# Kernel tuning notes

Hardware: AMD Instinct MI355X
Metric: run time of the kernel (lower is better)

The kernel has to match this reference:

```python
import jax, jax.numpy as jnp
import numpy as np

V, BLK, D, H, L = 50257, 2048, 768, 12, 4
HD = D // H
EPS = 1e-5


def _ln(x, w, b):
    mu = jnp.mean(x, axis=-1, keepdims=True)
    var = jnp.mean(jnp.square(x - mu), axis=-1, keepdims=True)
    return (x - mu) * jax.lax.rsqrt(var + EPS) * w + b


def setup_inputs() -> dict:
    key = jax.random.key(0)
    ks = iter(jax.random.split(key, 32))
    s = 0.02
    idx = jax.random.randint(next(ks), (2, 2048), 0, V)
    inp = {
        "idx": idx,
        "wte": jax.random.normal(next(ks), (V, D), jnp.float32) * s,
        "wpe": jax.random.normal(next(ks), (BLK, D), jnp.float32) * s,
        # stacked per-layer params [L, ...]
        "ln1_w": jnp.ones((L, D), jnp.float32),
        "ln1_b": jnp.zeros((L, D), jnp.float32),
        "attn_w": jax.random.normal(next(ks), (L, D, 3 * D), jnp.float32) * s,
        "attn_b": jnp.zeros((L, 3 * D), jnp.float32),
        "proj_w": jax.random.normal(next(ks), (L, D, D), jnp.float32) * (s / np.sqrt(2 * L)),
        "proj_b": jnp.zeros((L, D), jnp.float32),
        "ln2_w": jnp.ones((L, D), jnp.float32),
        "ln2_b": jnp.zeros((L, D), jnp.float32),
        "fc_w": jax.random.normal(next(ks), (L, D, 4 * D), jnp.float32) * s,
        "fc_b": jnp.zeros((L, 4 * D), jnp.float32),
        "fcp_w": jax.random.normal(next(ks), (L, 4 * D, D), jnp.float32) * (s / np.sqrt(2 * L)),
        "fcp_b": jnp.zeros((L, D), jnp.float32),
        "lnf_w": jnp.ones((D,), jnp.float32),
        "lnf_b": jnp.zeros((D,), jnp.float32),
    }
    return inp


def _gpt_forward(idx, wte, wpe, ln1_w, ln1_b, attn_w, attn_b, proj_w, proj_b,
                 ln2_w, ln2_b, fc_w, fc_b, fcp_w, fcp_b, lnf_w, lnf_b):
    B, T = idx.shape
    x = wte[idx] + wpe[:T]  # [B,T,D]; dropout p=0 -> identity
    causal = jnp.tril(jnp.ones((T, T), bool))
    scale = 1.0 / np.sqrt(HD)

    def block(x, p):
        l1w, l1b, aw, ab, pw, pb, l2w, l2b, fw, fb, fpw, fpb = p
        h = _ln(x, l1w, l1b)
        qkv = h @ aw + ab  # [B,T,3D]
        q, k, v = jnp.split(qkv, 3, axis=-1)
        q = q.reshape(B, T, H, HD).transpose(0, 2, 1, 3)  # [B,H,T,hd]
        k = k.reshape(B, T, H, HD).transpose(0, 2, 1, 3)
        v = v.reshape(B, T, H, HD).transpose(0, 2, 1, 3)
        att = jnp.einsum('bhqd,bhkd->bhqk', q, k) * scale
        att = jnp.where(causal, att, -jnp.inf)
        att = jax.nn.softmax(att, axis=-1)
        y = jnp.einsum('bhqk,bhkd->bhqd', att, v)
        y = y.transpose(0, 2, 1, 3).reshape(B, T, D)
        x = x + y @ pw + pb
        h2 = _ln(x, l2w, l2b)
        m = jax.nn.gelu(h2 @ fw + fb, approximate=False) @ fpw + fpb
        return x + m, None

    params = (ln1_w, ln1_b, attn_w, attn_b, proj_w, proj_b,
              ln2_w, ln2_b, fc_w, fc_b, fcp_w, fcp_b)
    x, _ = jax.lax.scan(block, x, params)
    x = _ln(x, lnf_w, lnf_b)
    # inference path: logits only for last position, lm_head tied to wte
    logits = x[:, -1:, :] @ wte.T  # [B,1,V]
    return logits


def reference(idx, wte, wpe, ln1_w, ln1_b, attn_w, attn_b, proj_w, proj_b,
              ln2_w, ln2_b, fc_w, fc_b, fcp_w, fcp_b, lnf_w, lnf_b):
    return _gpt_forward(idx, wte, wpe, ln1_w, ln1_b, attn_w, attn_b, proj_w, proj_b,
                        ln2_w, ln2_b, fc_w, fc_b, fcp_w, fcp_b, lnf_w, lnf_b)
```

## Files before the change

### kernel.cpp

```cpp
#include <hip/hip_runtime.h>
#include <math.h>

#define V 50257
#define B 2
#define T 2048
#define D 768
#define H 12
#define HD 64
#define L 4
#define D3 (3*D)
#define D4 (4*D)
#define NTOK (B*T)
#define EPS 1e-5f

typedef __bf16 v8bf __attribute__((ext_vector_type(8)));
typedef unsigned short v8us __attribute__((ext_vector_type(8)));
typedef float  v4f  __attribute__((ext_vector_type(4)));

#define GAS(p) ((const __attribute__((address_space(1))) void*)(p))
#define LAS(p) ((__attribute__((address_space(3))) void*)(p))

#define LIDX(row, chunk) ((row)*64 + ((((chunk) ^ ((row)&7)))<<3))

__global__ __launch_bounds__(256) void embed_kernel(const int* __restrict__ idx,
                                                    const float* __restrict__ wte,
                                                    const float* __restrict__ wpe,
                                                    float* __restrict__ x) {
    int i = blockIdx.x * 256 + threadIdx.x;
    if (i >= NTOK * D) return;
    int pos = i / D;
    int d   = i - pos * D;
    int t   = pos & (T - 1);
    int tok = idx[pos];
    x[i] = wte[tok * D + d] + wpe[t * D + d];
}

__global__ __launch_bounds__(256) void ln_kernel(const float* __restrict__ X,
                                                 const float* __restrict__ w,
                                                 const float* __restrict__ b,
                                                 __bf16* __restrict__ Y,
                                                 int src_mul, int src_off) {
    int srow = blockIdx.x * src_mul + src_off;
    const float* xr = X + (size_t)srow * D;
    float v[3];
    float s = 0.f, s2 = 0.f;
    #pragma unroll
    for (int j = 0; j < 3; ++j) {
        v[j] = xr[threadIdx.x + 256 * j];
        s += v[j];
        s2 += v[j] * v[j];
    }
    #pragma unroll
    for (int off = 32; off; off >>= 1) {
        s  += __shfl_xor(s, off);
        s2 += __shfl_xor(s2, off);
    }
    __shared__ float ss[4], ss2[4];
    int wave = threadIdx.x >> 6, lane = threadIdx.x & 63;
    if (lane == 0) { ss[wave] = s; ss2[wave] = s2; }
    __syncthreads();
    s  = ss[0] + ss[1] + ss[2] + ss[3];
    s2 = ss2[0] + ss2[1] + ss2[2] + ss2[3];
    float mu  = s * (1.f / D);
    float var = s2 * (1.f / D) - mu * mu;
    float rs  = rsqrtf(var + EPS);
    __bf16* yr = Y + (size_t)blockIdx.x * D;
    #pragma unroll
    for (int j = 0; j < 3; ++j) {
        int c = threadIdx.x + 256 * j;
        yr[c] = (__bf16)((v[j] - mu) * rs * w[c] + b[c]);
    }
}

__global__ __launch_bounds__(256) void convw4_kernel(
        const float* __restrict__ aw,  const float* __restrict__ pw,
        const float* __restrict__ fw,  const float* __restrict__ fpw,
        __bf16* __restrict__ awt, __bf16* __restrict__ pwt,
        __bf16* __restrict__ fwt, __bf16* __restrict__ fpwt) {
    int bid = blockIdx.x;
    const float* W; __bf16* Wt; int K, N, bx, by;
    if (bid < 1728)      {             W = aw;  Wt = awt;  K = D;  N = D3; bx = bid % 72; by = bid / 72; }
    else if (bid < 2304) { bid -= 1728; W = pw;  Wt = pwt;  K = D;  N = D;  bx = bid % 24; by = bid / 24; }
    else if (bid < 4608) { bid -= 2304; W = fw;  Wt = fwt;  K = D;  N = D4; bx = bid % 96; by = bid / 96; }
    else                 { bid -= 4608; W = fpw; Wt = fpwt; K = D4; N = D;  bx = bid % 24; by = bid / 24; }
    __shared__ float t[32][33];
    const int n0 = bx * 32, k0 = by * 32;
    const int tx = threadIdx.x & 31, ty = threadIdx.x >> 5;
    #pragma unroll
    for (int p = 0; p < 4; ++p)
        t[ty + 8 * p][tx] = W[(size_t)(k0 + ty + 8 * p) * N + n0 + tx];
    __syncthreads();
    #pragma unroll
    for (int p = 0; p < 4; ++p)
        Wt[(size_t)(n0 + ty + 8 * p) * K + k0 + tx] = (__bf16)t[tx][ty + 8 * p];
}

template<bool OUTBF16, bool DOGELU, bool DORES>
__global__ __launch_bounds__(256) void gemm_bt(const __bf16* __restrict__ A,
                                               const __bf16* __restrict__ Wt,
                                               const float* __restrict__ bias,
                                               const float* __restrict__ res,
                                               void* __restrict__ Cout,
                                               int N, int K) {
    __shared__ __align__(16) __bf16 As[4096];
    __shared__ __align__(16) __bf16 Bs[4096];
    const int tid  = threadIdx.x;
    const int w    = tid >> 6;
    const int lane = tid & 63;
    const int row0 = blockIdx.y * 128;
    const int col0 = blockIdx.x * 128;

    const int c0   = w * 64 + lane;
    const int srow = ((c0 >> 6) & 3) * 16 + (c0 & 15);
    const int sk   = ((c0 >> 4) & 3) * 8;
    const __bf16* gA0 = A  + (size_t)(row0 + srow) * K + sk;
    const __bf16* gA1 = gA0 + (size_t)64 * K;
    const __bf16* gB0 = Wt + (size_t)(col0 + srow) * K + sk;
    const __bf16* gB1 = gB0 + (size_t)64 * K;
    __bf16* lA0 = As + (size_t)c0 * 8;
    __bf16* lA1 = As + (size_t)(c0 + 256) * 8;
    __bf16* lB0 = Bs + (size_t)c0 * 8;
    __bf16* lB1 = Bs + (size_t)(c0 + 256) * 8;

    const int wr = w >> 1, wc = w & 1;
    const __bf16* rA = As + wr * 2048 + lane * 8;
    const __bf16* rB = Bs + wc * 2048 + lane * 8;

    v4f acc[4][4] = {};
    for (int k0 = 0; k0 < K; k0 += 32) {
        __builtin_amdgcn_global_load_lds(GAS(gA0), LAS(lA0), 16, 0, 0);
        __builtin_amdgcn_global_load_lds(GAS(gA1), LAS(lA1), 16, 0, 0);
        __builtin_amdgcn_global_load_lds(GAS(gB0), LAS(lB0), 16, 0, 0);
        __builtin_amdgcn_global_load_lds(GAS(gB1), LAS(lB1), 16, 0, 0);
        gA0 += 32; gA1 += 32; gB0 += 32; gB1 += 32;
        __syncthreads();
        v8bf af[4], bfr[4];
        #pragma unroll
        for (int i = 0; i < 4; ++i) af[i]  = *(const v8bf*)(rA + i * 512);
        #pragma unroll
        for (int j = 0; j < 4; ++j) bfr[j] = *(const v8bf*)(rB + j * 512);
        #pragma unroll
        for (int i = 0; i < 4; ++i)
            #pragma unroll
            for (int j = 0; j < 4; ++j)
                acc[i][j] = __builtin_amdgcn_mfma_f32_16x16x32_bf16(af[i], bfr[j], acc[i][j], 0, 0, 0);
        __syncthreads();
    }

    const int er = (lane >> 4) * 4;
    const int ec = lane & 15;
    #pragma unroll
    for (int j = 0; j < 4; ++j) {
        const int col = col0 + wc * 64 + j * 16 + ec;
        const float bval = bias[col];
        #pragma unroll
        for (int i = 0; i < 4; ++i) {
            #pragma unroll
            for (int rr = 0; rr < 4; ++rr) {
                const int row = row0 + wr * 64 + i * 16 + er + rr;
                float vv = acc[i][j][rr] + bval;
                if (DOGELU) vv = 0.5f * vv * (1.f + erff(vv * 0.70710678118f));
                if (DORES)  vv += res[(size_t)row * N + col];
                if (OUTBF16) ((__bf16*)Cout)[(size_t)row * N + col] = (__bf16)vv;
                else         ((float*) Cout)[(size_t)row * N + col] = vv;
            }
        }
    }
}

template<bool OUTBF16, bool DOGELU, bool DORES>
__global__ __launch_bounds__(256) void gemm_bt64(const __bf16* __restrict__ A,
                                                 const __bf16* __restrict__ Wt,
                                                 const float* __restrict__ bias,
                                                 const float* __restrict__ res,
                                                 void* __restrict__ Cout,
                                                 int N, int K) {
    __shared__ __align__(16) __bf16 As[4096];
    __shared__ __align__(16) __bf16 Bs[2048];
    const int tid  = threadIdx.x;
    const int w    = tid >> 6;
    const int lane = tid & 63;
    const int row0 = blockIdx.y * 128;
    const int col0 = blockIdx.x * 64;

    const int c0   = w * 64 + lane;
    const int srow = ((c0 >> 6) & 3) * 16 + (c0 & 15);
    const int sk   = ((c0 >> 4) & 3) * 8;
    const __bf16* gA0 = A  + (size_t)(row0 + srow) * K + sk;
    const __bf16* gA1 = gA0 + (size_t)64 * K;
    const __bf16* gB0 = Wt + (size_t)(col0 + srow) * K + sk;
    __bf16* lA0 = As + (size_t)c0 * 8;
    __bf16* lA1 = As + (size_t)(c0 + 256) * 8;
    __bf16* lB0 = Bs + (size_t)c0 * 8;

    const int wr = w >> 1, wc = w & 1;
    const __bf16* rA = As + wr * 2048 + lane * 8;
    const __bf16* rB = Bs + wc * 1024 + lane * 8;

    v4f acc[4][2] = {};
    for (int k0 = 0; k0 < K; k0 += 32) {
        __builtin_amdgcn_global_load_lds(GAS(gA0), LAS(lA0), 16, 0, 0);
        __builtin_amdgcn_global_load_lds(GAS(gA1), LAS(lA1), 16, 0, 0);
        __builtin_amdgcn_global_load_lds(GAS(gB0), LAS(lB0), 16, 0, 0);
        gA0 += 32; gA1 += 32; gB0 += 32;
        __syncthreads();
        v8bf af[4], bfr[2];
        #pragma unroll
        for (int i = 0; i < 4; ++i) af[i]  = *(const v8bf*)(rA + i * 512);
        #pragma unroll
        for (int j = 0; j < 2; ++j) bfr[j] = *(const v8bf*)(rB + j * 512);
        #pragma unroll
        for (int i = 0; i < 4; ++i)
            #pragma unroll
            for (int j = 0; j < 2; ++j)
                acc[i][j] = __builtin_amdgcn_mfma_f32_16x16x32_bf16(af[i], bfr[j], acc[i][j], 0, 0, 0);
        __syncthreads();
    }

    const int er = (lane >> 4) * 4;
    const int ec = lane & 15;
    #pragma unroll
    for (int j = 0; j < 2; ++j) {
        const int col = col0 + wc * 32 + j * 16 + ec;
        const float bval = bias[col];
        #pragma unroll
        for (int i = 0; i < 4; ++i) {
            #pragma unroll
            for (int rr = 0; rr < 4; ++rr) {
                const int row = row0 + wr * 64 + i * 16 + er + rr;
                float vv = acc[i][j][rr] + bval;
                if (DOGELU) vv = 0.5f * vv * (1.f + erff(vv * 0.70710678118f));
                if (DORES)  vv += res[(size_t)row * N + col];
                if (OUTBF16) ((__bf16*)Cout)[(size_t)row * N + col] = (__bf16)vv;
                else         ((float*) Cout)[(size_t)row * N + col] = vv;
            }
        }
    }
}

__global__ __launch_bounds__(256) void attn_mfma(const __bf16* __restrict__ qkv,
                                                 __bf16* __restrict__ y) {
    __shared__ __align__(16) __bf16 Qs[4096];
    __shared__ __align__(16) __bf16 Ks[4096];
    __shared__ __align__(16) __bf16 Vt[4096];
    __shared__ __align__(16) __bf16 Ps[4][1024];

    const int tid  = threadIdx.x;
    const int w    = tid >> 6;
    const int lane = tid & 63;
    const int quad = lane >> 4;
    const int l4   = lane & 15;

    const int qt = 31 - (blockIdx.x & 31);
    const int bh = blockIdx.x >> 5;
    const int b  = bh / H;
    const int h  = bh - b * H;
    const int q0 = qt * 64;

    const __bf16* base = qkv + (size_t)(b * T) * D3 + h * HD;

    {
        int c = tid;
        #pragma unroll
        for (int rep = 0; rep < 2; ++rep, c += 256) {
            int row = c >> 3, ch = c & 7;
            v8us v = *(const v8us*)(const void*)(base + (size_t)(q0 + row) * D3 + ch * 8);
            *(v8us*)(void*)(Qs + LIDX(row, ch)) = v;
        }
    }

    const int krow = tid >> 3, kch = tid & 7;
    const int vkp = tid & 31, vdc = tid >> 5;
    const __bf16* kp0 = base + D     + (size_t)krow * D3 + kch * 8;
    const __bf16* kp1 = kp0 + (size_t)32 * D3;
    const __bf16* vp0 = base + 2 * D + (size_t)(2 * vkp) * D3 + vdc * 8;
    const __bf16* vp1 = vp0 + D3;

    v8us kr0 = *(const v8us*)(const void*)kp0;
    v8us kr1 = *(const v8us*)(const void*)kp1;
    v8us vr0 = *(const v8us*)(const void*)vp0;
    v8us vr1 = *(const v8us*)(const void*)vp1;

    float m[4];
    #pragma unroll
    for (int i = 0; i < 4; ++i) m[i] = -INFINITY;
    v4f o[4] = {};
    v4f sacc = {};
    v8bf qf[2];
    v8bf vones;
    #pragma unroll
    for (int i = 0; i < 8; ++i) vones[i] = (__bf16)1.0f;

    const int nt = qt + 1;
    const size_t adv = (size_t)64 * D3;

    for (int kt = 0; kt < nt; ++kt) {
        const int k0 = kt * 64;
        *(v8us*)(void*)(Ks + LIDX(krow, kch))      = kr0;
        *(v8us*)(void*)(Ks + LIDX(krow + 32, kch)) = kr1;
        #pragma unroll
        for (int j = 0; j < 8; ++j) {
            int dim = vdc * 8 + j;
            int idx = dim * 64 + ((((vkp >> 2) ^ (dim & 7))) << 3) + ((vkp & 3) << 1);
            *(unsigned int*)(void*)(Vt + idx) =
                ((unsigned int)vr1[j] << 16) | (unsigned int)vr0[j];
        }
        __syncthreads();

        if (kt == 0) {
            #pragma unroll
            for (int kh = 0; kh < 2; ++kh)
                qf[kh] = *(const v8bf*)(Qs + LIDX(w * 16 + l4, kh * 4 + quad));
        }
        if (kt + 1 < nt) {
            kp0 += adv; kp1 += adv; vp0 += adv; vp1 += adv;
            kr0 = *(const v8us*)(const void*)kp0;
            kr1 = *(const v8us*)(const void*)kp1;
            vr0 = *(const v8us*)(const void*)vp0;
            vr1 = *(const v8us*)(const void*)vp1;
        }

        v4f s[4] = {};
        __builtin_amdgcn_s_setprio(1);
        #pragma unroll
        for (int kh = 0; kh < 2; ++kh) {
            #pragma unroll
            for (int jb = 0; jb < 4; ++jb) {
                v8bf bk = *(const v8bf*)(Ks + LIDX(jb * 16 + l4, kh * 4 + quad));
                s[jb] = __builtin_amdgcn_mfma_f32_16x16x32_bf16(qf[kh], bk, s[jb], 0, 0, 0);
            }
        }
        __builtin_amdgcn_s_setprio(0);

        float p[4][4];
        #pragma unroll
        for (int r = 0; r < 4; ++r) {
            const int qrow = q0 + w * 16 + quad * 4 + r;
            float svv[4];
            float mr = m[r];
            #pragma unroll
            for (int jb = 0; jb < 4; ++jb) {
                float sv = s[jb][r] * 0.125f;
                if (k0 + jb * 16 + l4 > qrow) sv = -INFINITY;
                svv[jb] = sv;
                mr = fmaxf(mr, sv);
            }
            #pragma unroll
            for (int off = 1; off < 16; off <<= 1) mr = fmaxf(mr, __shfl_xor(mr, off));
            const float alpha = __expf(m[r] - mr);
            m[r] = mr;
            #pragma unroll
            for (int jb = 0; jb < 4; ++jb) p[jb][r] = __expf(svv[jb] - mr);
            #pragma unroll
            for (int db = 0; db < 4; ++db) o[db][r] *= alpha;
            sacc[r] *= alpha;
        }
        #pragma unroll
        for (int jb = 0; jb < 4; ++jb) {
            #pragma unroll
            for (int r = 0; r < 4; ++r) {
                const int prow = quad * 4 + r;
                const int pidx = prow * 64 + ((((jb * 2 + (l4 >> 3)) ^ (prow & 7))) << 3) + (l4 & 7);
                Ps[w][pidx] = (__bf16)p[jb][r];
            }
        }
        __builtin_amdgcn_s_setprio(1);
        #pragma unroll
        for (int kh = 0; kh < 2; ++kh) {
            v8bf ap = *(const v8bf*)(&Ps[w][LIDX(l4, kh * 4 + quad)]);
            sacc = __builtin_amdgcn_mfma_f32_16x16x32_bf16(ap, vones, sacc, 0, 0, 0);
            #pragma unroll
            for (int db = 0; db < 4; ++db) {
                v8bf bv = *(const v8bf*)(Vt + LIDX(db * 16 + l4, kh * 4 + quad));
                o[db] = __builtin_amdgcn_mfma_f32_16x16x32_bf16(ap, bv, o[db], 0, 0, 0);
            }
        }
        __builtin_amdgcn_s_setprio(0);
        __syncthreads();
    }

    #pragma unroll
    for (int db = 0; db < 4; ++db) {
        #pragma unroll
        for (int r = 0; r < 4; ++r) {
            const int q = q0 + w * 16 + quad * 4 + r;
            y[(size_t)(b * T + q) * D + h * HD + db * 16 + l4] =
                (__bf16)(o[db][r] / sacc[r]);
        }
    }
}

__global__ __launch_bounds__(256) void logits_kernel(const __bf16* __restrict__ xf,
                                                     const float* __restrict__ wte,
                                                     float* __restrict__ out) {
    int wave = threadIdx.x >> 6;
    int lane = threadIdx.x & 63;
    int gid = blockIdx.x * 4 + wave;
    if (gid >= B * V) return;
    int b = gid / V;
    int v = gid - b * V;
    const float* wr = wte + (size_t)v * D;
    const __bf16* xr = xf + b * D;
    float s = 0.f;
    #pragma unroll
    for (int j = 0; j < 12; ++j)
        s = fmaf(wr[lane + 64 * j], (float)xr[lane + 64 * j], s);
    #pragma unroll
    for (int off = 32; off; off >>= 1) s += __shfl_xor(s, off);
    if (lane == 0) out[gid] = s;
}

extern "C" void kernel_launch(void* const* d_in, const int* in_sizes, int n_in,
                              void* d_out, int out_size, void* d_ws, size_t ws_size,
                              hipStream_t stream) {
    const int*   idx    = (const int*)  d_in[0];
    const float* wte    = (const float*)d_in[1];
    const float* wpe    = (const float*)d_in[2];
    const float* ln1_w  = (const float*)d_in[3];
    const float* ln1_b  = (const float*)d_in[4];
    const float* attn_w = (const float*)d_in[5];
    const float* attn_b = (const float*)d_in[6];
    const float* proj_w = (const float*)d_in[7];
    const float* proj_b = (const float*)d_in[8];
    const float* ln2_w  = (const float*)d_in[9];
    const float* ln2_b  = (const float*)d_in[10];
    const float* fc_w   = (const float*)d_in[11];
    const float* fc_b   = (const float*)d_in[12];
    const float* fcp_w  = (const float*)d_in[13];
    const float* fcp_b  = (const float*)d_in[14];
    const float* lnf_w  = (const float*)d_in[15];
    const float* lnf_b  = (const float*)d_in[16];
    float* out = (float*)d_out;

    char* ws = (char*)d_ws;
    float*  x    = (float*)ws;  ws += (size_t)NTOK * D  * 4;
    __bf16* qkvb = (__bf16*)ws;
    __bf16* gb   = (__bf16*)ws; ws += (size_t)NTOK * D4 * 2;
    __bf16* hb   = (__bf16*)ws; ws += (size_t)NTOK * D  * 2;
    __bf16* yb   = (__bf16*)ws; ws += (size_t)NTOK * D  * 2;
    __bf16* awt  = (__bf16*)ws; ws += (size_t)D3 * D   * 2;
    __bf16* pwt  = (__bf16*)ws; ws += (size_t)D  * D   * 2;
    __bf16* fwt  = (__bf16*)ws; ws += (size_t)D4 * D   * 2;
    __bf16* fpwt = (__bf16*)ws; ws += (size_t)D  * D4  * 2;
    __bf16* xf   = (__bf16*)ws; ws += (size_t)B * D    * 2;

    embed_kernel<<<(NTOK * D + 255) / 256, 256, 0, stream>>>(idx, wte, wpe, x);

    for (int l = 0; l < L; ++l) {
        const float* l1w = ln1_w + l * D;
        const float* l1b = ln1_b + l * D;
        const float* aw  = attn_w + (size_t)l * D * D3;
        const float* ab  = attn_b + l * D3;
        const float* pw  = proj_w + (size_t)l * D * D;
        const float* pb  = proj_b + l * D;
        const float* l2w = ln2_w + l * D;
        const float* l2b = ln2_b + l * D;
        const float* fw  = fc_w + (size_t)l * D * D4;
        const float* fb  = fc_b + l * D4;
        const float* fpw = fcp_w + (size_t)l * D4 * D;
        const float* fpb = fcp_b + l * D;

        convw4_kernel<<<6912, 256, 0, stream>>>(aw, pw, fw, fpw, awt, pwt, fwt, fpwt);

        ln_kernel<<<NTOK, 256, 0, stream>>>(x, l1w, l1b, hb, 1, 0);
        gemm_bt<true, false, false><<<dim3(D3 / 128, NTOK / 128), 256, 0, stream>>>(
            hb, awt, ab, nullptr, qkvb, D3, D);
        attn_mfma<<<B * H * (T / 64), 256, 0, stream>>>(qkvb, yb);
        gemm_bt64<false, false, true><<<dim3(D / 64, NTOK / 128), 256, 0, stream>>>(
            yb, pwt, pb, x, x, D, D);
        ln_kernel<<<NTOK, 256, 0, stream>>>(x, l2w, l2b, hb, 1, 0);
        gemm_bt<true, true, false><<<dim3(D4 / 128, NTOK / 128), 256, 0, stream>>>(
            hb, fwt, fb, nullptr, gb, D4, D);
        gemm_bt64<false, false, true><<<dim3(D / 64, NTOK / 128), 256, 0, stream>>>(
            gb, fpwt, fpb, x, x, D, D4);
    }

    ln_kernel<<<B, 256, 0, stream>>>(x, lnf_w, lnf_b, xf, T, T - 1);
    logits_kernel<<<(B * V + 3) / 4, 256, 0, stream>>>(xf, wte, out);
}
```

Measured before the change: 1.432 ms.

## Transpose QK^T in attention for per-lane softmax and batch weight conversion

The attention kernel swaps the MFMA operands so each lane holds scores for a single query row. The row max then needs only two cross-lane shuffles instead of four shuffles per row. P is written to shared memory as packed 4-element bf16 vectors, and the rescale factors are broadcast with shfl. Separately, the per-layer weight transpose/convert launches are merged into one launch covering all layers, which needs L times more workspace for the bf16 weights.

```diff
diff --git a/kernel.cpp b/kernel.cpp
--- a/kernel.cpp
+++ b/kernel.cpp
@@ -14,6 +14,7 @@
 #define EPS 1e-5f
 
 typedef __bf16 v8bf __attribute__((ext_vector_type(8)));
+typedef __bf16 v4bf __attribute__((ext_vector_type(4)));
 typedef unsigned short v8us __attribute__((ext_vector_type(8)));
 typedef float  v4f  __attribute__((ext_vector_type(4)));
 
@@ -73,16 +74,17 @@
 }
 
 __global__ __launch_bounds__(256) void convw4_kernel(
-        const float* __restrict__ aw,  const float* __restrict__ pw,
-        const float* __restrict__ fw,  const float* __restrict__ fpw,
-        __bf16* __restrict__ awt, __bf16* __restrict__ pwt,
-        __bf16* __restrict__ fwt, __bf16* __restrict__ fpwt) {
+        const float* __restrict__ aw_all,  const float* __restrict__ pw_all,
+        const float* __restrict__ fw_all,  const float* __restrict__ fpw_all,
+        __bf16* __restrict__ awt_all, __bf16* __restrict__ pwt_all,
+        __bf16* __restrict__ fwt_all, __bf16* __restrict__ fpwt_all) {
     int bid = blockIdx.x;
+    const int l = bid / 6912; bid -= l * 6912;
     const float* W; __bf16* Wt; int K, N, bx, by;
-    if (bid < 1728)      {             W = aw;  Wt = awt;  K = D;  N = D3; bx = bid % 72; by = bid / 72; }
-    else if (bid < 2304) { bid -= 1728; W = pw;  Wt = pwt;  K = D;  N = D;  bx = bid % 24; by = bid / 24; }
-    else if (bid < 4608) { bid -= 2304; W = fw;  Wt = fwt;  K = D;  N = D4; bx = bid % 96; by = bid / 96; }
-    else                 { bid -= 4608; W = fpw; Wt = fpwt; K = D4; N = D;  bx = bid % 24; by = bid / 24; }
+    if (bid < 1728)      {             W = aw_all  + (size_t)l * D  * D3; Wt = awt_all  + (size_t)l * D3 * D;  K = D;  N = D3; bx = bid % 72; by = bid / 72; }
+    else if (bid < 2304) { bid -= 1728; W = pw_all  + (size_t)l * D  * D;  Wt = pwt_all  + (size_t)l * D  * D;  K = D;  N = D;  bx = bid % 24; by = bid / 24; }
+    else if (bid < 4608) { bid -= 2304; W = fw_all  + (size_t)l * D  * D4; Wt = fwt_all  + (size_t)l * D4 * D;  K = D;  N = D4; bx = bid % 96; by = bid / 96; }
+    else                 { bid -= 4608; W = fpw_all + (size_t)l * D4 * D;  Wt = fpwt_all + (size_t)l * D  * D4; K = D4; N = D;  bx = bid % 24; by = bid / 24; }
     __shared__ float t[32][33];
     const int n0 = bx * 32, k0 = by * 32;
     const int tx = threadIdx.x & 31, ty = threadIdx.x >> 5;
@@ -281,9 +283,7 @@
     v8us vr0 = *(const v8us*)(const void*)vp0;
     v8us vr1 = *(const v8us*)(const void*)vp1;
 
-    float m[4];
-    #pragma unroll
-    for (int i = 0; i < 4; ++i) m[i] = -INFINITY;
+    float m_local = -INFINITY;
     v4f o[4] = {};
     v4f sacc = {};
     v8bf qf[2];
@@ -293,6 +293,7 @@
 
     const int nt = qt + 1;
     const size_t adv = (size_t)64 * D3;
+    const int qrow = q0 + w * 16 + l4;
 
     for (int kt = 0; kt < nt; ++kt) {
         const int k0 = kt * 64;
@@ -327,42 +328,44 @@
             #pragma unroll
             for (int jb = 0; jb < 4; ++jb) {
                 v8bf bk = *(const v8bf*)(Ks + LIDX(jb * 16 + l4, kh * 4 + quad));
-                s[jb] = __builtin_amdgcn_mfma_f32_16x16x32_bf16(qf[kh], bk, s[jb], 0, 0, 0);
+                s[jb] = __builtin_amdgcn_mfma_f32_16x16x32_bf16(bk, qf[kh], s[jb], 0, 0, 0);
             }
         }
         __builtin_amdgcn_s_setprio(0);
 
-        float p[4][4];
+        float sv[4][4];
+        float mx = -INFINITY;
+        #pragma unroll
+        for (int jb = 0; jb < 4; ++jb) {
+            #pragma unroll
+            for (int rg = 0; rg < 4; ++rg) {
+                float vvv = s[jb][rg] * 0.125f;
+                if (k0 + jb * 16 + quad * 4 + rg > qrow) vvv = -INFINITY;
+                sv[jb][rg] = vvv;
+                mx = fmaxf(mx, vvv);
+            }
+        }
+        mx = fmaxf(mx, __shfl_xor(mx, 16));
+        mx = fmaxf(mx, __shfl_xor(mx, 32));
+        const float mnew   = fmaxf(m_local, mx);
+        const float alpha_l = __expf(m_local - mnew);
+        m_local = mnew;
+        #pragma unroll
+        for (int jb = 0; jb < 4; ++jb) {
+            v4bf pk;
+            #pragma unroll
+            for (int rg = 0; rg < 4; ++rg)
+                pk[rg] = (__bf16)__expf(sv[jb][rg] - mnew);
+            *(v4bf*)(void*)(&Ps[w][LIDX(l4, jb * 2 + (quad >> 1)) + ((quad & 1) << 2)]) = pk;
+        }
+        float a4[4];
+        #pragma unroll
+        for (int r = 0; r < 4; ++r) a4[r] = __shfl(alpha_l, quad * 4 + r);
         #pragma unroll
         for (int r = 0; r < 4; ++r) {
-            const int qrow = q0 + w * 16 + quad * 4 + r;
-            float svv[4];
-            float mr = m[r];
-            #pragma unroll
-            for (int jb = 0; jb < 4; ++jb) {
-                float sv = s[jb][r] * 0.125f;
-                if (k0 + jb * 16 + l4 > qrow) sv = -INFINITY;
-                svv[jb] = sv;
-                mr = fmaxf(mr, sv);
-            }
-            #pragma unroll
-            for (int off = 1; off < 16; off <<= 1) mr = fmaxf(mr, __shfl_xor(mr, off));
-            const float alpha = __expf(m[r] - mr);
-            m[r] = mr;
-            #pragma unroll
-            for (int jb = 0; jb < 4; ++jb) p[jb][r] = __expf(svv[jb] - mr);
-            #pragma unroll
-            for (int db = 0; db < 4; ++db) o[db][r] *= alpha;
-            sacc[r] *= alpha;
-        }
-        #pragma unroll
-        for (int jb = 0; jb < 4; ++jb) {
-            #pragma unroll
-            for (int r = 0; r < 4; ++r) {
-                const int prow = quad * 4 + r;
-                const int pidx = prow * 64 + ((((jb * 2 + (l4 >> 3)) ^ (prow & 7))) << 3) + (l4 & 7);
-                Ps[w][pidx] = (__bf16)p[jb][r];
-            }
+            sacc[r] *= a4[r];
+            #pragma unroll
+            for (int db = 0; db < 4; ++db) o[db][r] *= a4[r];
         }
         __builtin_amdgcn_s_setprio(1);
         #pragma unroll
@@ -438,41 +441,42 @@
     __bf16* gb   = (__bf16*)ws; ws += (size_t)NTOK * D4 * 2;
     __bf16* hb   = (__bf16*)ws; ws += (size_t)NTOK * D  * 2;
     __bf16* yb   = (__bf16*)ws; ws += (size_t)NTOK * D  * 2;
-    __bf16* awt  = (__bf16*)ws; ws += (size_t)D3 * D   * 2;
-    __bf16* pwt  = (__bf16*)ws; ws += (size_t)D  * D   * 2;
-    __bf16* fwt  = (__bf16*)ws; ws += (size_t)D4 * D   * 2;
-    __bf16* fpwt = (__bf16*)ws; ws += (size_t)D  * D4  * 2;
+    __bf16* awt  = (__bf16*)ws; ws += (size_t)L * D3 * D   * 2;
+    __bf16* pwt  = (__bf16*)ws; ws += (size_t)L * D  * D   * 2;
+    __bf16* fwt  = (__bf16*)ws; ws += (size_t)L * D4 * D   * 2;
+    __bf16* fpwt = (__bf16*)ws; ws += (size_t)L * D  * D4  * 2;
     __bf16* xf   = (__bf16*)ws; ws += (size_t)B * D    * 2;
 
     embed_kernel<<<(NTOK * D + 255) / 256, 256, 0, stream>>>(idx, wte, wpe, x);
+
+    convw4_kernel<<<6912 * L, 256, 0, stream>>>(attn_w, proj_w, fc_w, fcp_w,
+                                                awt, pwt, fwt, fpwt);
 
     for (int l = 0; l < L; ++l) {
         const float* l1w = ln1_w + l * D;
         const float* l1b = ln1_b + l * D;
-        const float* aw  = attn_w + (size_t)l * D * D3;
         const float* ab  = attn_b + l * D3;
-        const float* pw  = proj_w + (size_t)l * D * D;
         const float* pb  = proj_b + l * D;
         const float* l2w = ln2_w + l * D;
         const float* l2b = ln2_b + l * D;
-        const float* fw  = fc_w + (size_t)l * D * D4;
         const float* fb  = fc_b + l * D4;
-        const float* fpw = fcp_w + (size_t)l * D4 * D;
         const float* fpb = fcp_b + l * D;
-
-        convw4_kernel<<<6912, 256, 0, stream>>>(aw, pw, fw, fpw, awt, pwt, fwt, fpwt);
+        const __bf16* awl  = awt  + (size_t)l * D3 * D;
+        const __bf16* pwl  = pwt  + (size_t)l * D  * D;
+        const __bf16* fwl  = fwt  + (size_t)l * D4 * D;
+        const __bf16* fpwl = fpwt + (size_t)l * D  * D4;
 
         ln_kernel<<<NTOK, 256, 0, stream>>>(x, l1w, l1b, hb, 1, 0);
         gemm_bt<true, false, false><<<dim3(D3 / 128, NTOK / 128), 256, 0, stream>>>(
-            hb, awt, ab, nullptr, qkvb, D3, D);
+            hb, awl, ab, nullptr, qkvb, D3, D);
         attn_mfma<<<B * H * (T / 64), 256, 0, stream>>>(qkvb, yb);
         gemm_bt64<false, false, true><<<dim3(D / 64, NTOK / 128), 256, 0, stream>>>(
-            yb, pwt, pb, x, x, D, D);
+            yb, pwl, pb, x, x, D, D);
         ln_kernel<<<NTOK, 256, 0, stream>>>(x, l2w, l2b, hb, 1, 0);
         gemm_bt<true, true, false><<<dim3(D4 / 128, NTOK / 128), 256, 0, stream>>>(
-            hb, fwt, fb, nullptr, gb, D4, D);
+            hb, fwl, fb, nullptr, gb, D4, D);
         gemm_bt64<false, false, true><<<dim3(D / 64, NTOK / 128), 256, 0, stream>>>(
-            gb, fpwt, fpb, x, x, D, D4);
+            gb, fpwl, fpb, x, x, D, D4);
     }
 
     ln_kernel<<<B, 256, 0, stream>>>(x, lnf_w, lnf_b, xf, T, T - 1);
```

Result: faster. 1.367 ms (-4.6%).
